# Optimization experiments

Measured on AMD Instinct MI355X. Metric: run time of the kernel, lower is better.

## Reference

```python
import jax, jax.numpy as jnp
import numpy as np

WS = 8      # window size
SS = 4      # shift size
NH = 4      # num heads
EPS = 1e-5
MLP_RATIO = 4


def _win_part(x, ws):
    # x: [B,D,H,W,C] -> [B*nD*nH*nW, ws^3, C]
    B, D, H, W, C = x.shape
    x = x.reshape(B, D // ws, ws, H // ws, ws, W // ws, ws, C)
    x = x.transpose(0, 1, 3, 5, 2, 4, 6, 7)
    return x.reshape(-1, ws * ws * ws, C)


def _win_rev(w, ws, B, D, H, W):
    C = w.shape[-1]
    x = w.reshape(B, D // ws, H // ws, W // ws, ws, ws, ws, C)
    x = x.transpose(0, 1, 4, 2, 5, 3, 6, 7)
    return x.reshape(B, D, H, W, C)


def _ln(x, g, b):
    m = jnp.mean(x, axis=-1, keepdims=True)
    v = jnp.mean((x - m) ** 2, axis=-1, keepdims=True)
    return (x - m) / jnp.sqrt(v + EPS) * g + b


def _rel_index(ws):
    coords = np.stack(np.meshgrid(np.arange(ws), np.arange(ws), np.arange(ws), indexing='ij'))  # [3,ws,ws,ws]
    cf = coords.reshape(3, -1)                      # [3, ws^3]
    rel = (cf[:, :, None] - cf[:, None, :]).transpose(1, 2, 0) + (ws - 1)  # [N,N,3]
    return rel[..., 0] * (2 * ws - 1) ** 2 + rel[..., 1] * (2 * ws - 1) + rel[..., 2]


def _attn_mask(D, H, W, ws, ss):
    img = np.zeros((1, D, H, W, 1), dtype=np.float32)
    cnt = 0
    sl = (slice(0, -ws), slice(-ws, -ss), slice(-ss, None))
    for d in sl:
        for h in sl:
            for w in sl:
                img[:, d, h, w, :] = cnt
                cnt += 1
    mw = np.asarray(_win_part(jnp.asarray(img), ws))[..., 0]  # [nW, ws^3]
    diff = mw[:, None, :] - mw[:, :, None]
    return np.where(diff != 0, -100.0, 0.0).astype(np.float32)


def setup_inputs() -> dict:
    key = jax.random.key(0)
    ks = jax.random.split(key, 12)
    B, D, H, W, C = 1, 16, 64, 64, 128
    mh = MLP_RATIO * C
    s = 0.02
    return {
        'x': jax.random.normal(ks[0], (B, D, H, W, C), jnp.float32),
        'attn_mask': jnp.asarray(_attn_mask(D, H, W, WS, SS)),
        'rel_index': jnp.asarray(_rel_index(WS), jnp.int32),
        'rel_bias': jax.random.normal(ks[1], ((2 * WS - 1) ** 3, NH), jnp.float32) * s,
        'qkv_w': jax.random.normal(ks[2], (3 * C, C), jnp.float32) * s,
        'qkv_b': jnp.zeros((3 * C,), jnp.float32),
        'proj_w': jax.random.normal(ks[3], (C, C), jnp.float32) * s,
        'proj_b': jnp.zeros((C,), jnp.float32),
        'norm1_g': jnp.ones((C,), jnp.float32),
        'norm1_b': jnp.zeros((C,), jnp.float32),
        'norm2_g': jnp.ones((C,), jnp.float32),
        'norm2_b': jnp.zeros((C,), jnp.float32),
        'mlp_w1': jax.random.normal(ks[4], (mh, C), jnp.float32) * s,
        'mlp_b1': jnp.zeros((mh,), jnp.float32),
        'mlp_w2': jax.random.normal(ks[5], (C, mh), jnp.float32) * s,
        'mlp_b2': jnp.zeros((C,), jnp.float32),
    }


def reference(x, attn_mask, rel_index, rel_bias, qkv_w, qkv_b, proj_w, proj_b,
              norm1_g, norm1_b, norm2_g, norm2_b, mlp_w1, mlp_b1, mlp_w2, mlp_b2):
    B, D, H, W, C = x.shape
    ws, ss, nh = WS, SS, NH
    hd = C // nh
    scale = hd ** -0.5
    N = ws ** 3
    shortcut = x
    h = _ln(x, norm1_g, norm1_b)
    h = jnp.roll(h, (-ss, -ss, -ss), axis=(1, 2, 3))
    xw = _win_part(h, ws)                 # [B_, N, C]
    B_ = xw.shape[0]
    nW = attn_mask.shape[0]
    qkv = xw @ qkv_w.T + qkv_b            # [B_, N, 3C]
    qkv = qkv.reshape(B_, N, 3, nh, hd).transpose(2, 0, 3, 1, 4)  # [3,B_,h,N,hd]
    q, k, v = qkv[0] * scale, qkv[1], qkv[2]
    attn = jnp.einsum('bhnd,bhmd->bhnm', q, k)
    rpe = rel_bias[rel_index.reshape(-1)].reshape(N, N, nh).transpose(2, 0, 1)  # [h,N,N]
    attn = attn + rpe[None]
    attn = attn.reshape(B_ // nW, nW, nh, N, N) + attn_mask[None, :, None]
    attn = jax.nn.softmax(attn.reshape(B_, nh, N, N), axis=-1)
    out = jnp.einsum('bhnm,bhmd->bhnd', attn, v).transpose(0, 2, 1, 3).reshape(B_, N, C)
    out = out @ proj_w.T + proj_b
    out = _win_rev(out, ws, B, D, H, W)
    out = jnp.roll(out, (ss, ss, ss), axis=(1, 2, 3))
    x = shortcut + out
    h2 = _ln(x, norm2_g, norm2_b)
    h2 = jax.nn.gelu(h2 @ mlp_w1.T + mlp_b1, approximate=False)
    return x + h2 @ mlp_w2.T + mlp_b2
```

## Files before the change

kernel.cpp:

```cpp
#include <hip/hip_runtime.h>
#include <math.h>

typedef __bf16 bf16;
typedef __bf16 bf16x4 __attribute__((ext_vector_type(4)));
typedef __bf16 bf16x8 __attribute__((ext_vector_type(8)));
typedef float f32x4 __attribute__((ext_vector_type(4)));
typedef unsigned short u16;
typedef u16 u16x2 __attribute__((ext_vector_type(2)));

#define LOG2E 1.4426950408889634f

__device__ __forceinline__ float b2f(u16 b) {
  return (float)__builtin_bit_cast(bf16, b);
}

__global__ void sniff_k(const unsigned* __restrict__ xw_, int* __restrict__ flag) {
  int lane = threadIdx.x;
  int c = 0;
#pragma unroll
  for (int j = 0; j < 4; j++) {
    unsigned e = (xw_[lane * 4 + j] >> 7) & 0xFFu;
    c += (e >= 100u && e <= 140u) ? 1 : 0;
  }
#pragma unroll
  for (int d = 1; d < 64; d <<= 1) c += __shfl_xor(c, d);
  if (lane == 0) *flag = (c >= 150) ? 1 : 0;
}

__global__ __launch_bounds__(256) void canon_big_k(const void* __restrict__ src,
                                                   bf16* __restrict__ dst,
                                                   const int* __restrict__ flag) {
  int i = (blockIdx.x * 256 + threadIdx.x) * 8;
  if (*flag) {
    *(bf16x8*)&dst[i] = *(const bf16x8*)((const bf16*)src + i);
  } else {
    const float* s = (const float*)src + i;
    bf16x8 v;
#pragma unroll
    for (int j = 0; j < 8; j++) v[j] = (bf16)s[j];
    *(bf16x8*)&dst[i] = v;
  }
}

struct CanonArgs {
  const void* src[13];
  bf16* dst[13];
  int n[13];
};

__global__ __launch_bounds__(256) void canon_small_k(CanonArgs a,
                                                     const int* __restrict__ flag) {
  int ti = blockIdx.y;
  int i = blockIdx.x * 256 + threadIdx.x;
  if (i >= a.n[ti]) return;
  if (*flag)
    a.dst[ti][i] = ((const bf16*)a.src[ti])[i];
  else
    a.dst[ti][i] = (bf16)((const float*)a.src[ti])[i];
}

__global__ __launch_bounds__(256) void rpem_k(const int* __restrict__ ridx,
                                              const bf16* __restrict__ rbias,
                                              bf16* __restrict__ rpem) {
  int t = blockIdx.x * 256 + threadIdx.x;
  int m0 = (t & 127) * 4, q = (t >> 7) & 511, h = (t >> 16) & 3, ty = t >> 18;
  int qd = q >> 6, qh = (q >> 3) & 7, qw = q & 7;
  int4 ri = *(const int4*)&ridx[q * 512 + m0];
  const int rv[4] = {ri.x, ri.y, ri.z, ri.w};
  bf16x4 o;
#pragma unroll
  for (int j = 0; j < 4; j++) {
    int m = m0 + j;
    int md = m >> 6, mh = (m >> 3) & 7, mw = m & 7;
    bool diff = ((ty & 4) && ((qd < 4) != (md < 4))) ||
                ((ty & 2) && ((qh < 4) != (mh < 4))) ||
                ((ty & 1) && ((qw < 4) != (mw < 4)));
    float v = (float)rbias[rv[j] * 4 + h] * LOG2E;
    o[j] = (bf16)(v + (diff ? -144.2695041f : 0.f));
  }
  *(bf16x4*)&rpem[(size_t)t * 4] = o;
}

template <int ROLL>
__global__ __launch_bounds__(256) void ln_k(const bf16* __restrict__ x,
                                            const bf16* __restrict__ g,
                                            const bf16* __restrict__ bsh,
                                            bf16* __restrict__ out) {
  int wave = threadIdx.x >> 6, lane = threadIdx.x & 63;
  int tok = blockIdx.x * 4 + wave;
  size_t src;
  if (ROLL) {
    int win = tok >> 9, pos = tok & 511;
    int rd = (win >> 6) * 8 + (pos >> 6);
    int rh = ((win >> 3) & 7) * 8 + ((pos >> 3) & 7);
    int rw = (win & 7) * 8 + (pos & 7);
    int od = (rd + 4) & 15, oh = (rh + 4) & 63, ow = (rw + 4) & 63;
    src = (size_t)((od * 64 + oh) * 64 + ow) * 128;
  } else {
    src = (size_t)tok * 128;
  }
  int ch = lane * 2;
  u16x2 xv = *(const u16x2*)(x + src + ch);
  float f0 = b2f(xv[0]), f1 = b2f(xv[1]);
  float s = f0 + f1, sq = f0 * f0 + f1 * f1;
#pragma unroll
  for (int d = 1; d < 64; d <<= 1) {
    s += __shfl_xor(s, d);
    sq += __shfl_xor(sq, d);
  }
  float mean = s * (1.f / 128.f);
  float var = sq * (1.f / 128.f) - mean * mean;
  float rstd = rsqrtf(fmaxf(var, 0.f) + 1e-5f);
  u16x2 gv = *(const u16x2*)(g + ch), bv = *(const u16x2*)(bsh + ch);
  u16x2 ov;
  ov[0] = __builtin_bit_cast(u16, (bf16)((f0 - mean) * rstd * b2f(gv[0]) + b2f(bv[0])));
  ov[1] = __builtin_bit_cast(u16, (bf16)((f1 - mean) * rstd * b2f(gv[1]) + b2f(bv[1])));
  *(u16x2*)(out + (size_t)tok * 128 + ch) = ov;
}

template <int EPI, int BM, int N_, int K_>
__global__ __launch_bounds__(256) void gemm_k(const bf16* __restrict__ A,
                                              const bf16* __restrict__ B,
                                              const bf16* __restrict__ bias,
                                              void* __restrict__ outv,
                                              const bf16* __restrict__ resid,
                                              const int* __restrict__ flag) {
  __shared__ __align__(16) u16 As[BM * 72];
  __shared__ __align__(16) u16 Bs[128 * 72];
  const int t = threadIdx.x;
  const int wave = t >> 6, lane = t & 63, l15 = lane & 15, quad = lane >> 4;
  const int m0 = blockIdx.x * BM, n0 = blockIdx.y * 128;
  constexpr int MI = BM / 32;
  constexpr int PA = BM / 32;
  int fl = 0;
  if constexpr (EPI == 3) fl = *flag;
  f32x4 acc[MI][4] = {};
  const int wr = (wave >> 1) * (BM / 2), wc = (wave & 1) * 64;
  const int srow = t >> 3, scol = (t & 7) * 8;
  constexpr int NC = K_ / 64;
  bf16x8 avA[PA], avB[PA];
#pragma unroll
  for (int p = 0; p < PA; p++) {
    int row = p * 32 + srow;
    avA[p] = *(const bf16x8*)(A + (size_t)(m0 + row) * K_ + scol);
  }
#pragma unroll
  for (int c = 0; c < NC; c++) {
    const bf16x8* av = (c & 1) ? avB : avA;
    bf16x8* avN = (c & 1) ? avA : avB;
    if (c + 1 < NC) {
#pragma unroll
      for (int p = 0; p < PA; p++) {
        int row = p * 32 + srow;
        avN[p] = *(const bf16x8*)(A + (size_t)(m0 + row) * K_ + (c + 1) * 64 + scol);
      }
    }
    bf16x8 bv[4];
#pragma unroll
    for (int p = 0; p < 4; p++) {
      int row = p * 32 + srow;
      bv[p] = *(const bf16x8*)(B + (size_t)(n0 + row) * K_ + c * 64 + scol);
    }
    __syncthreads();
#pragma unroll
    for (int p = 0; p < PA; p++)
      *(bf16x8*)&As[(p * 32 + srow) * 72 + scol] = av[p];
#pragma unroll
    for (int p = 0; p < 4; p++)
      *(bf16x8*)&Bs[(p * 32 + srow) * 72 + scol] = bv[p];
    __syncthreads();
#pragma unroll
    for (int ks = 0; ks < 2; ks++) {
      bf16x8 a[MI], b[4];
#pragma unroll
      for (int i = 0; i < MI; i++)
        a[i] = *(const bf16x8*)&As[(wr + i * 16 + l15) * 72 + ks * 32 + quad * 8];
#pragma unroll
      for (int j = 0; j < 4; j++)
        b[j] = *(const bf16x8*)&Bs[(wc + j * 16 + l15) * 72 + ks * 32 + quad * 8];
#pragma unroll
      for (int i = 0; i < MI; i++)
#pragma unroll
        for (int j = 0; j < 4; j++)
          acc[i][j] =
              __builtin_amdgcn_mfma_f32_16x16x32_bf16(a[i], b[j], acc[i][j], 0, 0, 0);
    }
  }
  const float qscale = 0.17677669529663687f * LOG2E;
#pragma unroll
  for (int i = 0; i < MI; i++) {
#pragma unroll
    for (int r = 0; r < 4; r++) {
      int tok = m0 + wr + i * 16 + quad * 4 + r;
      size_t obase = 0;
      if constexpr (EPI == 1) {
        int win = tok >> 9, pos = tok & 511;
        int rd = (win >> 6) * 8 + (pos >> 6);
        int rh = ((win >> 3) & 7) * 8 + ((pos >> 3) & 7);
        int rw = (win & 7) * 8 + (pos & 7);
        int od = (rd + 4) & 15, oh = (rh + 4) & 63, ow = (rw + 4) & 63;
        obase = (size_t)((od * 64 + oh) * 64 + ow) * 128;
      } else if constexpr (EPI != 0) {
        obase = (size_t)tok * N_;
      }
#pragma unroll
      for (int j = 0; j < 4; j++) {
        int gn = n0 + wc + j * 16 + l15;
        float v = acc[i][j][r] + (float)bias[gn];
        if constexpr (EPI == 0) {
          int tensor = gn >> 7, c = gn & 127, head = c >> 5, d = c & 31;
          if (tensor == 0) v *= qscale;
          int win = tok >> 9, pos = tok & 511;
          size_t off = ((((size_t)tensor * 4 + head) * 128 + win) * 512 + pos) * 32 + d;
          ((bf16*)outv)[off] = (bf16)v;
        } else if constexpr (EPI == 1) {
          v += (float)resid[obase + gn];
          ((bf16*)outv)[obase + gn] = (bf16)v;
        } else if constexpr (EPI == 2) {
          float v2 = v * v;
          float u2 = v * (2.30220806f + 0.10294323f * v2);
          float e2 = exp2f(u2);
          float rcp = __builtin_amdgcn_rcpf(e2 + 1.f);
          v = v - v * rcp;
          ((bf16*)outv)[obase + gn] = (bf16)v;
        } else {
          v += (float)resid[obase + gn];
          if (fl)
            ((bf16*)outv)[obase + gn] = (bf16)v;
          else
            ((float*)outv)[obase + gn] = v;
        }
      }
    }
  }
}

__global__ __launch_bounds__(256) void attn_k(const bf16* __restrict__ qkv,
                                              const bf16* __restrict__ rpem,
                                              bf16* __restrict__ att) {
  __shared__ __align__(16) bf16 sVt[32 * 520];
  __shared__ __align__(16) bf16 sP[4][32 * 72];
  const int t = threadIdx.x;
  const int p = blockIdx.x;
  const int win = ((p >> 7) << 3) | (p & 7);
  const int j = (p >> 3) & 15;
  const int head = j >> 2, qc = j & 3;
  const int wave = t >> 6, lane = t & 63, l15 = lane & 15, quad = lane >> 4;

  const int wd = win >> 6, wh = (win >> 3) & 7, ww = win & 7;
  const int type = ((wd == 1) << 2) | ((wh == 7) << 1) | (ww == 7);

  const size_t hw32 = (size_t)512 * 32;
  const bf16* qp = qkv + ((size_t)(0 * 4 + head) * 128 + win) * hw32;
  const bf16* kp = qkv + ((size_t)(1 * 4 + head) * 128 + win) * hw32;
  const bf16* vp = qkv + ((size_t)(2 * 4 + head) * 128 + win) * hw32;
  const bf16* rpeh = rpem + (size_t)(type * 4 + head) * 512 * 512;
  const int qbase = qc * 128 + wave * 32;

  {
    int kpi = t >> 3, dblk = (t & 7) * 4;
    unsigned* s32 = (unsigned*)sVt;
#pragma unroll
    for (int kb = 0; kb < 8; kb++) {
      const bf16* v0 = vp + (size_t)(kb * 64 + 2 * kpi) * 32 + dblk;
      bf16x4 a = *(const bf16x4*)v0;
      bf16x4 b = *(const bf16x4*)(v0 + 32);
      int keyw = (kb * 64 + 2 * kpi) >> 1;
#pragma unroll
      for (int dd = 0; dd < 4; dd++) {
        unsigned wv = (unsigned)__builtin_bit_cast(u16, a[dd]) |
                      ((unsigned)__builtin_bit_cast(u16, b[dd]) << 16);
        s32[(dblk + dd) * 260 + keyw] = wv;
      }
    }
  }

  bf16x8 qa[2];
#pragma unroll
  for (int nt = 0; nt < 2; nt++)
    qa[nt] = *(const bf16x8*)(qp + (size_t)(qbase + nt * 16 + l15) * 32 + quad * 8);

  __syncthreads();

  f32x4 O[2][2] = {};
  float ls[2] = {0.f, 0.f};
  bf16* pw = sP[wave];

  bf16x8 kb[4];
  bf16x4 rv[4][2];
#pragma unroll
  for (int mt = 0; mt < 4; mt++) {
    kb[mt] = *(const bf16x8*)(kp + (size_t)(mt * 16 + l15) * 32 + quad * 8);
#pragma unroll
    for (int nt = 0; nt < 2; nt++)
      rv[mt][nt] = *(const bf16x4*)(rpeh + (size_t)(qbase + nt * 16 + l15) * 512 +
                                    mt * 16 + quad * 4);
  }

  for (int kt = 0; kt < 8; kt++) {
    bf16x8 kbn[4];
    bf16x4 rvn[4][2];
    if (kt < 7) {
#pragma unroll
      for (int mt = 0; mt < 4; mt++) {
        kbn[mt] = *(const bf16x8*)(kp +
                                   (size_t)((kt + 1) * 64 + mt * 16 + l15) * 32 +
                                   quad * 8);
#pragma unroll
        for (int nt = 0; nt < 2; nt++)
          rvn[mt][nt] =
              *(const bf16x4*)(rpeh + (size_t)(qbase + nt * 16 + l15) * 512 +
                               (kt + 1) * 64 + mt * 16 + quad * 4);
      }
    }
    f32x4 S[4][2];
#pragma unroll
    for (int mt = 0; mt < 4; mt++)
#pragma unroll
      for (int nt = 0; nt < 2; nt++) {
        f32x4 c;
#pragma unroll
        for (int r = 0; r < 4; r++) c[r] = (float)rv[mt][nt][r];
        S[mt][nt] = __builtin_amdgcn_mfma_f32_16x16x32_bf16(kb[mt], qa[nt], c, 0, 0, 0);
      }
#pragma unroll
    for (int nt = 0; nt < 2; nt++)
#pragma unroll
      for (int mt = 0; mt < 4; mt++) {
        bf16x4 pv;
#pragma unroll
        for (int r = 0; r < 4; r++) {
          float pe = exp2f(S[mt][nt][r]);
          ls[nt] += pe;
          pv[r] = (bf16)pe;
        }
        *(bf16x4*)&pw[(nt * 16 + l15) * 72 + mt * 16 + quad * 4] = pv;
      }
#pragma unroll
    for (int s = 0; s < 2; s++) {
      bf16x8 va0 = *(const bf16x8*)&sVt[l15 * 520 + kt * 64 + s * 32 + quad * 8];
      bf16x8 va1 =
          *(const bf16x8*)&sVt[(16 + l15) * 520 + kt * 64 + s * 32 + quad * 8];
      bf16x8 pb0 = *(const bf16x8*)&pw[l15 * 72 + s * 32 + quad * 8];
      bf16x8 pb1 = *(const bf16x8*)&pw[(16 + l15) * 72 + s * 32 + quad * 8];
      O[0][0] = __builtin_amdgcn_mfma_f32_16x16x32_bf16(va0, pb0, O[0][0], 0, 0, 0);
      O[0][1] = __builtin_amdgcn_mfma_f32_16x16x32_bf16(va0, pb1, O[0][1], 0, 0, 0);
      O[1][0] = __builtin_amdgcn_mfma_f32_16x16x32_bf16(va1, pb0, O[1][0], 0, 0, 0);
      O[1][1] = __builtin_amdgcn_mfma_f32_16x16x32_bf16(va1, pb1, O[1][1], 0, 0, 0);
    }
#pragma unroll
    for (int mt = 0; mt < 4; mt++) {
      kb[mt] = kbn[mt];
      rv[mt][0] = rvn[mt][0];
      rv[mt][1] = rvn[mt][1];
    }
  }
#pragma unroll
  for (int nt = 0; nt < 2; nt++) {
    float l = ls[nt];
    l += __shfl_xor(l, 16);
    l += __shfl_xor(l, 32);
    float inv = __builtin_amdgcn_rcpf(l);
    int q = qbase + nt * 16 + l15;
#pragma unroll
    for (int dm = 0; dm < 2; dm++) {
      bf16x4 o;
#pragma unroll
      for (int r = 0; r < 4; r++) o[r] = (bf16)(O[dm][nt][r] * inv);
      *(bf16x4*)(att + ((size_t)win * 512 + q) * 128 + head * 32 + dm * 16 +
                 quad * 4) = o;
    }
  }
}

extern "C" void kernel_launch(void* const* d_in, const int* in_sizes, int n_in,
                              void* d_out, int out_size, void* d_ws,
                              size_t ws_size, hipStream_t stream) {
  const int* rel_index = (const int*)d_in[2];
  char* w = (char*)d_ws;

  int* flag = (int*)w;
  bf16* rb_c = (bf16*)(w + (64ull << 10));
  bf16* qw_c = (bf16*)(w + (128ull << 10));
  bf16* pw_c = (bf16*)(w + (256ull << 10));
  bf16* w1_c = (bf16*)(w + (320ull << 10));
  bf16* w2_c = (bf16*)(w + (512ull << 10));
  bf16* qb_c = (bf16*)(w + (704ull << 10));
  bf16* pb_c = (bf16*)(w + (708ull << 10));
  bf16* g1_c = (bf16*)(w + (712ull << 10));
  bf16* b1n_c = (bf16*)(w + (716ull << 10));
  bf16* g2_c = (bf16*)(w + (720ull << 10));
  bf16* b2n_c = (bf16*)(w + (724ull << 10));
  bf16* mb1_c = (bf16*)(w + (728ull << 10));
  bf16* mb2_c = (bf16*)(w + (732ull << 10));
  bf16* x_c = (bf16*)(w + (1ull << 20));
  bf16* xw = (bf16*)(w + (17ull << 20));
  bf16* qkvb = (bf16*)(w + (33ull << 20));
  bf16* x2 = (bf16*)(w + (99ull << 20));
  bf16* rpem = x2;
  bf16* att = xw;
  bf16* h2 = xw;
  bf16* a1 = qkvb;

  sniff_k<<<1, 64, 0, stream>>>((const unsigned*)d_in[0], flag);
  canon_big_k<<<4096, 256, 0, stream>>>(d_in[0], x_c, flag);

  CanonArgs ca;
  const int srcidx[13] = {3, 4, 5, 6, 7, 8, 9, 10, 11, 12, 13, 14, 15};
  bf16* dsts[13] = {rb_c, qw_c, qb_c, pw_c, pb_c, g1_c, b1n_c,
                    g2_c, b2n_c, w1_c, mb1_c, w2_c, mb2_c};
  for (int i = 0; i < 13; i++) {
    ca.src[i] = d_in[srcidx[i]];
    ca.dst[i] = dsts[i];
    ca.n[i] = in_sizes[srcidx[i]];
  }
  canon_small_k<<<dim3(256, 13), 256, 0, stream>>>(ca, flag);

  rpem_k<<<8192, 256, 0, stream>>>(rel_index, rb_c, rpem);
  ln_k<1><<<16384, 256, 0, stream>>>(x_c, g1_c, b1n_c, xw);
  gemm_k<0, 128, 384, 128><<<dim3(512, 3), 256, 0, stream>>>(xw, qw_c, qb_c,
                                                             qkvb, nullptr, flag);
  attn_k<<<2048, 256, 0, stream>>>(qkvb, rpem, att);
  gemm_k<1, 64, 128, 128><<<dim3(1024, 1), 256, 0, stream>>>(att, pw_c, pb_c,
                                                             x2, x_c, flag);
  ln_k<0><<<16384, 256, 0, stream>>>(x2, g2_c, b2n_c, h2);
  gemm_k<2, 128, 512, 128><<<dim3(512, 4), 256, 0, stream>>>(h2, w1_c, mb1_c,
                                                             a1, nullptr, flag);
  gemm_k<3, 64, 128, 512><<<dim3(1024, 1), 256, 0, stream>>>(a1, w2_c, mb2_c,
                                                             d_out, x2, flag);
}
```

Baseline: 414.0 us.

## Double attention block size and replace LDS padding with XOR swizzle

The attention kernel now runs 512 threads per block covering half of a window's queries for one head, instead of 256 threads covering a quarter. This halves how often each window's V tile is transposed and staged into shared memory. Row padding for the shared V and P tiles is replaced by an XOR swizzle to avoid bank conflicts with a denser layout. The barrier now comes after the initial K and bias loads, and the key loop is fully unrolled. Risks are lower occupancy from larger blocks and higher register pressure from the unroll.

```diff
diff --git a/kernel.cpp b/kernel.cpp
--- a/kernel.cpp
+++ b/kernel.cpp
@@ -235,16 +235,16 @@
   }
 }
 
-__global__ __launch_bounds__(256) void attn_k(const bf16* __restrict__ qkv,
+__global__ __launch_bounds__(512) void attn_k(const bf16* __restrict__ qkv,
                                               const bf16* __restrict__ rpem,
                                               bf16* __restrict__ att) {
-  __shared__ __align__(16) bf16 sVt[32 * 520];
-  __shared__ __align__(16) bf16 sP[4][32 * 72];
+  __shared__ __align__(16) bf16 sVt[32 * 512];
+  __shared__ __align__(16) bf16 sP[8][32 * 64];
   const int t = threadIdx.x;
   const int p = blockIdx.x;
-  const int win = ((p >> 7) << 3) | (p & 7);
-  const int j = (p >> 3) & 15;
-  const int head = j >> 2, qc = j & 3;
+  const int win = ((p >> 6) << 3) | (p & 7);
+  const int mid = (p >> 3) & 7;
+  const int head = mid >> 1, qh = mid & 1;
   const int wave = t >> 6, lane = t & 63, l15 = lane & 15, quad = lane >> 4;
 
   const int wd = win >> 6, wh = (win >> 3) & 7, ww = win & 7;
@@ -255,22 +255,23 @@
   const bf16* kp = qkv + ((size_t)(1 * 4 + head) * 128 + win) * hw32;
   const bf16* vp = qkv + ((size_t)(2 * 4 + head) * 128 + win) * hw32;
   const bf16* rpeh = rpem + (size_t)(type * 4 + head) * 512 * 512;
-  const int qbase = qc * 128 + wave * 32;
+  const int qbase = qh * 256 + wave * 32;
 
   {
     int kpi = t >> 3, dblk = (t & 7) * 4;
-    unsigned* s32 = (unsigned*)sVt;
-#pragma unroll
-    for (int kb = 0; kb < 8; kb++) {
-      const bf16* v0 = vp + (size_t)(kb * 64 + 2 * kpi) * 32 + dblk;
+    char* sb = (char*)sVt;
+#pragma unroll
+    for (int kb = 0; kb < 4; kb++) {
+      const bf16* v0 = vp + (size_t)(kb * 128 + 2 * kpi) * 32 + dblk;
       bf16x4 a = *(const bf16x4*)v0;
       bf16x4 b = *(const bf16x4*)(v0 + 32);
-      int keyw = (kb * 64 + 2 * kpi) >> 1;
+      int keyw = kb * 64 + kpi;
 #pragma unroll
       for (int dd = 0; dd < 4; dd++) {
+        int row = dblk + dd;
         unsigned wv = (unsigned)__builtin_bit_cast(u16, a[dd]) |
                       ((unsigned)__builtin_bit_cast(u16, b[dd]) << 16);
-        s32[(dblk + dd) * 260 + keyw] = wv;
+        *(unsigned*)(sb + ((row * 1024 + keyw * 4) ^ ((row & 7) << 4))) = wv;
       }
     }
   }
@@ -279,12 +280,6 @@
 #pragma unroll
   for (int nt = 0; nt < 2; nt++)
     qa[nt] = *(const bf16x8*)(qp + (size_t)(qbase + nt * 16 + l15) * 32 + quad * 8);
-
-  __syncthreads();
-
-  f32x4 O[2][2] = {};
-  float ls[2] = {0.f, 0.f};
-  bf16* pw = sP[wave];
 
   bf16x8 kb[4];
   bf16x4 rv[4][2];
@@ -297,6 +292,15 @@
                                     mt * 16 + quad * 4);
   }
 
+  __syncthreads();
+
+  f32x4 O[2][2] = {};
+  float ls[2] = {0.f, 0.f};
+  char* pw = (char*)sP[wave];
+  const char* sv = (const char*)sVt;
+  const int swz = (l15 & 7) << 4;
+
+#pragma unroll
   for (int kt = 0; kt < 8; kt++) {
     bf16x8 kbn[4];
     bf16x4 rvn[4][2];
@@ -334,15 +338,16 @@
           ls[nt] += pe;
           pv[r] = (bf16)pe;
         }
-        *(bf16x4*)&pw[(nt * 16 + l15) * 72 + mt * 16 + quad * 4] = pv;
+        *(bf16x4*)(pw + (((nt * 16 + l15) * 128 + mt * 32 + quad * 8) ^ swz)) = pv;
       }
 #pragma unroll
     for (int s = 0; s < 2; s++) {
-      bf16x8 va0 = *(const bf16x8*)&sVt[l15 * 520 + kt * 64 + s * 32 + quad * 8];
-      bf16x8 va1 =
-          *(const bf16x8*)&sVt[(16 + l15) * 520 + kt * 64 + s * 32 + quad * 8];
-      bf16x8 pb0 = *(const bf16x8*)&pw[l15 * 72 + s * 32 + quad * 8];
-      bf16x8 pb1 = *(const bf16x8*)&pw[(16 + l15) * 72 + s * 32 + quad * 8];
+      int vc = kt * 128 + s * 64 + quad * 16;
+      int pc = s * 64 + quad * 16;
+      bf16x8 va0 = *(const bf16x8*)(sv + ((l15 * 1024 + vc) ^ swz));
+      bf16x8 va1 = *(const bf16x8*)(sv + (((16 + l15) * 1024 + vc) ^ swz));
+      bf16x8 pb0 = *(const bf16x8*)(pw + ((l15 * 128 + pc) ^ swz));
+      bf16x8 pb1 = *(const bf16x8*)(pw + (((16 + l15) * 128 + pc) ^ swz));
       O[0][0] = __builtin_amdgcn_mfma_f32_16x16x32_bf16(va0, pb0, O[0][0], 0, 0, 0);
       O[0][1] = __builtin_amdgcn_mfma_f32_16x16x32_bf16(va0, pb1, O[0][1], 0, 0, 0);
       O[1][0] = __builtin_amdgcn_mfma_f32_16x16x32_bf16(va1, pb0, O[1][0], 0, 0, 0);
@@ -420,7 +425,7 @@
   ln_k<1><<<16384, 256, 0, stream>>>(x_c, g1_c, b1n_c, xw);
   gemm_k<0, 128, 384, 128><<<dim3(512, 3), 256, 0, stream>>>(xw, qw_c, qb_c,
                                                              qkvb, nullptr, flag);
-  attn_k<<<2048, 256, 0, stream>>>(qkvb, rpem, att);
+  attn_k<<<1024, 512, 0, stream>>>(qkvb, rpem, att);
   gemm_k<1, 64, 128, 128><<<dim3(1024, 1), 256, 0, stream>>>(att, pw_c, pb_c,
                                                              x2, x_c, flag);
   ln_k<0><<<16384, 256, 0, stream>>>(x2, g2_c, b2n_c, h2);
```

Result: slower. 461.6 us (+11.5%).
